# Optimization experiments

Hardware: AMD Instinct MI355X
Metric: run time of the kernel (lower is better)

The kernel has to match this reference:

```python
import jax, jax.numpy as jnp
import numpy as np

C = 1.0          # curvature
TOP_K = 5
LAMBDA_H = 0.01
TAU = 0.1        # forward default
NEG_SAMPLES = 20 # forward default
EPS = 1e-9
B, D = 4096, 64


def _to_ball(v):
    # map gaussian vectors strictly inside the unit Poincare ball
    return 0.8 * v / (1.0 + jnp.linalg.norm(v, axis=-1, keepdims=True))


def setup_inputs() -> dict:
    key = jax.random.key(0)
    ka, kt = jax.random.split(key)
    audio = _to_ball(jax.random.normal(ka, (B, D), dtype=jnp.float32))
    text = _to_ball(jax.random.normal(kt, (B, D), dtype=jnp.float32))
    return {"audio_embeds": audio, "text_embeds": text}


def _pairwise_poincare(x, y, c=C):
    # ||x-y||^2 via gemm instead of materializing [N,N,D] diff tensor
    x_sq = jnp.sum(x * x, axis=-1, keepdims=True)          # [N,1]
    y_sq = jnp.sum(y * y, axis=-1, keepdims=True).T        # [1,M]
    diff_sq = jnp.maximum(x_sq + y_sq - 2.0 * (x @ y.T), 0.0)
    x_cl = jnp.minimum(x_sq, 1.0 - EPS)
    y_cl = jnp.minimum(y_sq, 1.0 - EPS)
    denom = jnp.maximum((1.0 - x_cl) * (1.0 - y_cl), EPS)
    z = jnp.maximum(1.0 + 2.0 * diff_sq / denom, 1.0 + EPS)
    return jnp.arccosh(z) / jnp.sqrt(jnp.asarray(c, x.dtype))


def _topk_triplet(embeds, key):
    n = embeds.shape[0]
    dist = _pairwise_poincare(embeds, embeds)
    dist = dist.at[jnp.arange(n), jnp.arange(n)].set(jnp.inf)  # fill_diagonal_(inf)
    k = min(TOP_K, n - 1)
    neg_pos, pos_idx = jax.lax.top_k(-dist, k)                 # k smallest distances
    pos_term = jax.scipy.special.logsumexp(neg_pos / TAU, axis=1)  # logsumexp(-pos_dist/tau)
    # mask out top-k positives (diagonal stays in pool, holding +inf -> exp(-inf)=0)
    mask = jnp.ones((n, n), bool).at[jnp.arange(n)[:, None], pos_idx].set(False)
    # stable argsort: mask-True columns first, in original column order -> matches dist[i][mask[i]]
    order = jnp.argsort(jnp.where(mask, 0, 1), axis=1)
    pool = jnp.take_along_axis(dist, order[:, : n - k], axis=1)    # [n, n-k]
    samp = jax.random.randint(key, (n, NEG_SAMPLES), 0, n - k)
    neg_vals = jnp.take_along_axis(pool, samp, axis=1)             # [n, NEG_SAMPLES]
    neg_term = jax.scipy.special.logsumexp(-neg_vals / TAU, axis=1)
    return jnp.mean(neg_term - pos_term)  # mean of -(pos_term - neg_term)


def reference(audio_embeds, text_embeds):
    # HyperbolicLayeredLoss.forward returns lambda_h * (text_h + audio_h);
    # the cross-modal loss is computed but NOT added to the returned total in the source.
    key_text = jax.random.key(1)
    key_audio = jax.random.key(2)
    loss_text_h = _topk_triplet(text_embeds, key_text)
    loss_audio_h = _topk_triplet(audio_embeds, key_audio)
    return LAMBDA_H * (loss_text_h + loss_audio_h)
```

## Files before the change

kernel.cpp:

```cpp
#include <hip/hip_runtime.h>
#include <stdint.h>

#define JAX_PARTITIONABLE 1

constexpr int N = 4096;
constexpr int DIM = 64;
constexpr int TOPK = 5;
constexpr int NEGS = 20;
constexpr float TAU_ = 0.1f;
constexpr uint32_t SPAN = 4091u;
constexpr uint32_t MULT = 2309u;

constexpr int CQ = 256;
constexpr int NQ = N / CQ;
constexpr int NT = CQ / 16;
constexpr int RPB = 64;
constexpr int YSTRIDE = 136;

typedef __attribute__((ext_vector_type(8))) short bf16x8;
typedef __attribute__((ext_vector_type(4))) float f32x4;

__device__ __forceinline__ uint32_t rotl32(uint32_t v, int d) {
  return (v << d) | (v >> (32 - d));
}

__device__ __forceinline__ void threefry(uint32_t k0, uint32_t k1,
                                         uint32_t& x0, uint32_t& x1) {
  const uint32_t k2 = k0 ^ k1 ^ 0x1BD11BDAu;
  x0 += k0; x1 += k1;
#define TF_R(r) { x0 += x1; x1 = rotl32(x1, r); x1 ^= x0; }
  TF_R(13) TF_R(15) TF_R(26) TF_R(6)
  x0 += k1; x1 += k2 + 1u;
  TF_R(17) TF_R(29) TF_R(16) TF_R(24)
  x0 += k2; x1 += k0 + 2u;
  TF_R(13) TF_R(15) TF_R(26) TF_R(6)
  x0 += k0; x1 += k1 + 3u;
  TF_R(17) TF_R(29) TF_R(16) TF_R(24)
  x0 += k1; x1 += k2 + 4u;
  TF_R(13) TF_R(15) TF_R(26) TF_R(6)
  x0 += k2; x1 += k0 + 5u;
#undef TF_R
}

__device__ __forceinline__ uint32_t sample_idx(uint32_t seed, uint32_t f) {
#if JAX_PARTITIONABLE
  uint32_t a0 = 0u, a1 = 0u; threefry(0u, seed, a0, a1);
  uint32_t b0 = 0u, b1 = 1u; threefry(0u, seed, b0, b1);
  uint32_t h0 = 0u, h1 = f;  threefry(a0, a1, h0, h1);
  const uint32_t hi = h0 ^ h1;
  uint32_t l0 = 0u, l1 = f;  threefry(b0, b1, l0, l1);
  const uint32_t lo = l0 ^ l1;
#else
  uint32_t a0 = 0u, a1 = 2u; threefry(0u, seed, a0, a1);
  uint32_t c0 = 1u, c1 = 3u; threefry(0u, seed, c0, c1);
  const uint32_t HALF = (uint32_t)(N * NEGS / 2);
  uint32_t hi, lo;
  if (f < HALF) {
    uint32_t x0 = f, x1 = f + HALF; threefry(a0, c0, x0, x1); hi = x0;
    x0 = f; x1 = f + HALF;          threefry(a1, c1, x0, x1); lo = x0;
  } else {
    uint32_t x0 = f - HALF, x1 = f; threefry(a0, c0, x0, x1); hi = x1;
    x0 = f - HALF; x1 = f;          threefry(a1, c1, x0, x1); lo = x1;
  }
#endif
  return ((hi % SPAN) * MULT + (lo % SPAN)) % SPAN;
}

__device__ __forceinline__ float acosh_dev(float z) {
  return logf(z + sqrtf((z - 1.0f) * (z + 1.0f)));
}

__device__ __forceinline__ uint16_t f2bf(float f) {
  const uint32_t u = __float_as_uint(f);
  return (uint16_t)((u + 0x7FFFu + ((u >> 16) & 1u)) >> 16);
}
__device__ __forceinline__ float bf2f(uint16_t h) {
  return __uint_as_float((uint32_t)h << 16);
}

__global__ __launch_bounds__(64) void k_pre(const float* __restrict__ Xa,
                                            const float* __restrict__ Xt,
                                            uint16_t* __restrict__ Xs,
                                            float* __restrict__ ysq,
                                            float* __restrict__ inv) {
  const int m = blockIdx.y;
  const float* __restrict__ X = (m == 0) ? Xt : Xa;
  const int i = blockIdx.x * 64 + threadIdx.x;
  const float* xr = X + (size_t)i * DIM;

  uint32_t hb[DIM / 2], lb[DIM / 2];
  float s = 0.0f;
#pragma unroll
  for (int u = 0; u < DIM / 4; ++u) {
    const float4 v = *(const float4*)(xr + 4 * u);
    s = fmaf(v.x, v.x, s); s = fmaf(v.y, v.y, s);
    s = fmaf(v.z, v.z, s); s = fmaf(v.w, v.w, s);
    const uint16_t h0 = f2bf(v.x), h1 = f2bf(v.y), h2 = f2bf(v.z), h3 = f2bf(v.w);
    const uint16_t l0 = f2bf(v.x - bf2f(h0)), l1 = f2bf(v.y - bf2f(h1));
    const uint16_t l2 = f2bf(v.z - bf2f(h2)), l3 = f2bf(v.w - bf2f(h3));
    hb[2 * u]     = (uint32_t)h0 | ((uint32_t)h1 << 16);
    hb[2 * u + 1] = (uint32_t)h2 | ((uint32_t)h3 << 16);
    lb[2 * u]     = (uint32_t)l0 | ((uint32_t)l1 << 16);
    lb[2 * u + 1] = (uint32_t)l2 | ((uint32_t)l3 << 16);
  }
  uint32_t* dst = (uint32_t*)(Xs + (size_t)(m * N + i) * 128);
#pragma unroll
  for (int w = 0; w < 8; ++w) {
    uint4 qh = { hb[4 * w], hb[4 * w + 1], hb[4 * w + 2], hb[4 * w + 3] };
    ((uint4*)dst)[w] = qh;
  }
#pragma unroll
  for (int w = 0; w < 8; ++w) {
    uint4 ql = { lb[4 * w], lb[4 * w + 1], lb[4 * w + 2], lb[4 * w + 3] };
    ((uint4*)dst)[8 + w] = ql;
  }
  ysq[m * N + i] = s;
  inv[m * N + i] = 1.0f / (1.0f - fminf(s, 1.0f));
}

__global__ __launch_bounds__(256) void k_top5(
    const uint16_t* __restrict__ Xs, const float* __restrict__ ysq,
    const float* __restrict__ inv, uint64_t* __restrict__ partial) {
  const int lin = (int)blockIdx.x;
  const int wg = ((lin & 7) << 8) | (lin >> 3);
  const int m = wg >> 10;
  const int qq = (wg >> 6) & 15;
  const int rb = wg & 63;

  const int tid = (int)threadIdx.x;
  const int wid = tid >> 6;
  const int l = tid & 63;
  const int i0w = rb * RPB + wid * 16;
  const int j0q = qq * CQ;
  const int mN = m * N;
  const uint16_t* __restrict__ Xm = Xs + (size_t)m * N * 128;
  const int lc = l & 15;
  const int lk = l >> 4;
  const int lk4 = lk * 4;
  const int lk8 = lk * 8;
  const int sr = tid >> 4;
  const int sc8 = (tid & 15) * 8;

  __shared__ __align__(16) unsigned char smem[2 * 16 * YSTRIDE * 2 + 2048];
  uint16_t* y0 = (uint16_t*)smem;
  uint16_t* y1 = y0 + 16 * YSTRIDE;
  float* sq_s = (float*)(smem + 2 * 16 * YSTRIDE * 2);
  float* iv_s = sq_s + CQ;

  bf16x8 xf[2][2];
#pragma unroll
  for (int c = 0; c < 2; ++c)
#pragma unroll
    for (int h = 0; h < 2; ++h)
      xf[c][h] = *(const bf16x8*)(Xm + (size_t)(i0w + lc) * 128 +
                                  h * 64 + c * 32 + lk8);

  const float xsq_i = ysq[mN + i0w + lc];
  const float inv2_i = 2.0f * inv[mN + i0w + lc];
  const int gi = i0w + lc;

  const uint64_t SENT = ((uint64_t)0x7F800000u << 32) | 0xFFFFFFFFu;
  uint64_t t5[TOPK];
#pragma unroll
  for (int t = 0; t < TOPK; ++t) t5[t] = SENT;

  const f32x4 zz = {0.0f, 0.0f, 0.0f, 0.0f};
  const float INF_ = __uint_as_float(0x7F800000u);

  {
    if (tid < 64)
      *(float4*)&sq_s[tid * 4] = *(const float4*)&ysq[mN + j0q + tid * 4];
    else if (tid < 128)
      *(float4*)&iv_s[(tid - 64) * 4] =
          *(const float4*)&inv[mN + j0q + (tid - 64) * 4];
    const uint4 s0 =
        *(const uint4*)(Xm + (size_t)(j0q + sr) * 128 + sc8);
    *(uint4*)(y0 + sr * YSTRIDE + sc8) = s0;
    __syncthreads();
  }

#pragma unroll 1
  for (int T = 0; T < NT; ++T) {
    const bool have_next = (T + 1 < NT);
    uint4 stg;
    if (have_next)
      stg = *(const uint4*)(Xm + (size_t)(j0q + (T + 1) * 16 + sr) * 128 + sc8);

    const uint16_t* yp = ((T & 1) ? y1 : y0) + lc * YSTRIDE + lk8;
    const bf16x8 Y0 = *(const bf16x8*)(yp);
    const bf16x8 Y1 = *(const bf16x8*)(yp + 32);
    const bf16x8 Y2 = *(const bf16x8*)(yp + 64);
    const bf16x8 Y3 = *(const bf16x8*)(yp + 96);

    f32x4 acc;
    acc = __builtin_amdgcn_mfma_f32_16x16x32_bf16(Y0, xf[0][0], zz, 0, 0, 0);
    acc = __builtin_amdgcn_mfma_f32_16x16x32_bf16(Y1, xf[1][0], acc, 0, 0, 0);
    acc = __builtin_amdgcn_mfma_f32_16x16x32_bf16(Y2, xf[0][0], acc, 0, 0, 0);
    acc = __builtin_amdgcn_mfma_f32_16x16x32_bf16(Y3, xf[1][0], acc, 0, 0, 0);
    acc = __builtin_amdgcn_mfma_f32_16x16x32_bf16(Y0, xf[0][1], acc, 0, 0, 0);
    acc = __builtin_amdgcn_mfma_f32_16x16x32_bf16(Y1, xf[1][1], acc, 0, 0, 0);

    const float4 sq4 = *(const float4*)&sq_s[T * 16 + lk4];
    const float4 iv4 = *(const float4*)&iv_s[T * 16 + lk4];
    const int jb = j0q + T * 16;

    float w_ = __uint_as_float((uint32_t)(t5[TOPK - 1] >> 32));
    w_ = fminf(w_, __shfl_xor(w_, 16, 64));
    const float tau_ = fminf(w_, __shfl_xor(w_, 32, 64));

    float zt[4];
#pragma unroll
    for (int p = 0; p < 4; ++p) {
      const float yc = (p == 0) ? sq4.x : (p == 1) ? sq4.y
                      : (p == 2) ? sq4.z : sq4.w;
      const float ic = (p == 0) ? iv4.x : (p == 1) ? iv4.y
                      : (p == 2) ? iv4.z : iv4.w;
      const float diff = fmaxf(xsq_i + yc - 2.0f * acc[p], 0.0f);
      zt[p] = fmaf(diff * inv2_i, ic, 1.0f);
    }
    if (jb == i0w) {
#pragma unroll
      for (int p = 0; p < 4; ++p)
        if (gi == jb + lk4 + p) zt[p] = INF_;
    }
    const float zm = fminf(fminf(zt[0], zt[1]), fminf(zt[2], zt[3]));
    if (zm <= tau_) {
#pragma unroll
      for (int p = 0; p < 4; ++p) {
        uint64_t key = ((uint64_t)__float_as_uint(zt[p]) << 32) |
                       (uint32_t)(jb + lk4 + p);
        if (key < t5[TOPK - 1]) {
#pragma unroll
          for (int tt = 0; tt < TOPK; ++tt) {
            const uint64_t cv = t5[tt];
            if (key < cv) { t5[tt] = key; key = cv; }
          }
        }
      }
    }

    if (have_next)
      *(uint4*)(((T & 1) ? y0 : y1) + sr * YSTRIDE + sc8) = stg;
    __syncthreads();
  }

  uint64_t* mb = (uint64_t*)smem;
#pragma unroll
  for (int t = 0; t < TOPK; ++t)
    mb[((size_t)(wid * 16) + lc) * 21 + lk * TOPK + t] = t5[t];
  __syncthreads();

  if (l < 16) {
    uint64_t cur[TOPK];
#pragma unroll
    for (int t = 0; t < TOPK; ++t) cur[t] = mb[((size_t)(wid * 16) + l) * 21 + t];
    for (int c = 1; c < 4; ++c) {
      for (int t = 0; t < TOPK; ++t) {
        uint64_t key = mb[((size_t)(wid * 16) + l) * 21 + c * TOPK + t];
        if (key >= cur[TOPK - 1]) break;
#pragma unroll
        for (int u = 0; u < TOPK; ++u) {
          const uint64_t cv = cur[u];
          if (key < cv) { cur[u] = key; key = cv; }
        }
      }
    }
#pragma unroll
    for (int t = 0; t < TOPK; ++t)
      partial[((size_t)(m * NQ + qq) * N + i0w + l) * TOPK + t] = cur[t];
  }
}

__global__ __launch_bounds__(64) void k_neg(const float* __restrict__ Xa,
                                            const float* __restrict__ Xt,
                                            const float* __restrict__ ysq,
                                            const float* __restrict__ inv,
                                            const uint64_t* __restrict__ partial,
                                            float* __restrict__ rowres) {
  const int m = blockIdx.y;
  const int i = blockIdx.x;
  const float* __restrict__ X = (m == 0) ? Xt : Xa;
  const uint32_t seed = (m == 0) ? 1u : 2u;
  const int lane = threadIdx.x;

  __shared__ float4 xi4[DIM / 4];
  __shared__ float posv[TOPK];
  if (lane < DIM / 4) xi4[lane] = ((const float4*)(X + (size_t)i * DIM))[lane];
  __syncthreads();

  uint64_t cur[TOPK];
#pragma unroll
  for (int t = 0; t < TOPK; ++t)
    cur[t] = partial[((size_t)(m * NQ) * N + i) * TOPK + t];
  for (int q = 1; q < NQ; ++q) {
    for (int t = 0; t < TOPK; ++t) {
      uint64_t key = partial[((size_t)(m * NQ + q) * N + i) * TOPK + t];
      if (key >= cur[TOPK - 1]) break;
#pragma unroll
      for (int u = 0; u < TOPK; ++u) {
        const uint64_t cv = cur[u];
        if (key < cv) { cur[u] = key; key = cv; }
      }
    }
  }

  const float ysq_i = ysq[m * N + i];
  const float inv_i = inv[m * N + i];

  if (lane >= 32 && lane < 32 + TOPK) {
    const int t = lane - 32;
    const uint32_t c = (uint32_t)(cur[t] & 0xffffffffu);
    const float4* xc = (const float4*)(X + (size_t)c * DIM);
    float dot = 0.0f;
#pragma unroll
    for (int k = 0; k < DIM / 4; ++k) {
      const float4 a = xi4[k];
      const float4 b = xc[k];
      dot = fmaf(a.x, b.x, dot); dot = fmaf(a.y, b.y, dot);
      dot = fmaf(a.z, b.z, dot); dot = fmaf(a.w, b.w, dot);
    }
    const float diff = fmaxf(ysq_i + ysq[m * N + c] - 2.0f * dot, 0.0f);
    const float z = 1.0f + 2.0f * diff * inv_i * inv[m * N + c];
    posv[t] = -acosh_dev(z) / TAU_;
  }

  uint32_t pidx[TOPK];
#pragma unroll
  for (int t = 0; t < TOPK; ++t) pidx[t] = (uint32_t)(cur[t] & 0xffffffffu);

#define CSWAP(a, b)                                                           \
  { const uint32_t mn = pidx[a] < pidx[b] ? pidx[a] : pidx[b];                \
    const uint32_t mx = pidx[a] < pidx[b] ? pidx[b] : pidx[a];                \
    pidx[a] = mn; pidx[b] = mx; }
  CSWAP(0, 1) CSWAP(3, 4) CSWAP(2, 4) CSWAP(2, 3) CSWAP(1, 4)
  CSWAP(0, 3) CSWAP(0, 2) CSWAP(1, 3) CSWAP(1, 2)
#undef CSWAP

  float v = -1e30f;
  if (lane < NEGS) {
    const uint32_t f = (uint32_t)i * (uint32_t)NEGS + (uint32_t)lane;
    uint32_t c = sample_idx(seed, f);
#pragma unroll
    for (int t = 0; t < TOPK; ++t) c += (c >= pidx[t]) ? 1u : 0u;
    if (c != (uint32_t)i) {
      const float4* xc = (const float4*)(X + (size_t)c * DIM);
      float dot = 0.0f;
#pragma unroll
      for (int k = 0; k < DIM / 4; ++k) {
        const float4 a = xi4[k];
        const float4 b = xc[k];
        dot = fmaf(a.x, b.x, dot); dot = fmaf(a.y, b.y, dot);
        dot = fmaf(a.z, b.z, dot); dot = fmaf(a.w, b.w, dot);
      }
      const float diff = fmaxf(ysq_i + ysq[m * N + c] - 2.0f * dot, 0.0f);
      const float z = 1.0f + 2.0f * diff * inv_i * inv[m * N + c];
      v = -acosh_dev(z) / TAU_;
    }
  }

  __syncthreads();

  float vmax = v;
#pragma unroll
  for (int o = 32; o > 0; o >>= 1) vmax = fmaxf(vmax, __shfl_xor(vmax, o, 64));
  float e = expf(v - vmax);
  float ss = e;
#pragma unroll
  for (int o = 32; o > 0; o >>= 1) ss += __shfl_xor(ss, o, 64);

  if (lane == 0) {
    float vm = -1e30f;
#pragma unroll
    for (int t = 0; t < TOPK; ++t) vm = fmaxf(vm, posv[t]);
    float ps = 0.0f;
#pragma unroll
    for (int t = 0; t < TOPK; ++t) ps += expf(posv[t] - vm);
    const float pos = vm + logf(ps);
    rowres[m * N + i] = (vmax + logf(ss)) - pos;
  }
}

__global__ __launch_bounds__(256) void k_reduce(const float* __restrict__ rowres,
                                                float* __restrict__ out) {
  __shared__ double sh[256];
  double s = 0.0;
  for (int idx = threadIdx.x; idx < 2 * N; idx += 256) s += (double)rowres[idx];
  sh[threadIdx.x] = s;
  __syncthreads();
  for (int o = 128; o > 0; o >>= 1) {
    if (threadIdx.x < o) sh[threadIdx.x] += sh[threadIdx.x + o];
    __syncthreads();
  }
  if (threadIdx.x == 0) out[0] = (float)(0.01 * (sh[0] / (double)N));
}

extern "C" void kernel_launch(void* const* d_in, const int* in_sizes, int n_in,
                              void* d_out, int out_size, void* d_ws,
                              size_t ws_size, hipStream_t stream) {
  const float* Xa = (const float*)d_in[0];
  const float* Xt = (const float*)d_in[1];
  float* out = (float*)d_out;

  float* ysq = (float*)d_ws;
  float* inv = ysq + 2 * N;
  uint64_t* partial = (uint64_t*)(inv + 2 * N);
  float* rowres = (float*)(partial + (size_t)2 * NQ * N * TOPK);
  uint16_t* Xs = (uint16_t*)(rowres + 2 * N);

  k_pre<<<dim3(N / 64, 2), 64, 0, stream>>>(Xa, Xt, Xs, ysq, inv);
  k_top5<<<(N / RPB) * NQ * 2, 256, 0, stream>>>(Xs, ysq, inv, partial);
  k_neg<<<dim3(N, 2), 64, 0, stream>>>(Xa, Xt, ysq, inv, partial, rowres);
  k_reduce<<<1, 256, 0, stream>>>(rowres, out);
}
```

Measured before the change: 107.1 us.

## Process two Y tiles per barrier and use per-lane top-k threshold

Grows the shared-memory Y staging from two to four 16-row buffers so each loop iteration handles two tiles and prefetches the next two, halving the number of __syncthreads calls. It also replaces the cross-lane shuffle-reduced pruning threshold with a per-lane threshold that is updated only after insertions, which removes two shuffles per tile. A per-lane threshold is looser than the min across lanes, so more candidates may reach the insertion sort. The larger LDS footprint could also lower occupancy.

```diff
diff --git a/kernel.cpp b/kernel.cpp
--- a/kernel.cpp
+++ b/kernel.cpp
@@ -141,10 +141,9 @@
   const int sr = tid >> 4;
   const int sc8 = (tid & 15) * 8;
 
-  __shared__ __align__(16) unsigned char smem[2 * 16 * YSTRIDE * 2 + 2048];
-  uint16_t* y0 = (uint16_t*)smem;
-  uint16_t* y1 = y0 + 16 * YSTRIDE;
-  float* sq_s = (float*)(smem + 2 * 16 * YSTRIDE * 2);
+  __shared__ __align__(16) unsigned char smem[4 * 16 * YSTRIDE * 2 + 2048];
+  uint16_t* ybuf = (uint16_t*)smem;
+  float* sq_s = (float*)(smem + 4 * 16 * YSTRIDE * 2);
   float* iv_s = sq_s + CQ;
 
   bf16x8 xf[2][2];
@@ -163,6 +162,7 @@
   uint64_t t5[TOPK];
 #pragma unroll
   for (int t = 0; t < TOPK; ++t) t5[t] = SENT;
+  float z5own = __uint_as_float(0x7F800000u);
 
   const f32x4 zz = {0.0f, 0.0f, 0.0f, 0.0f};
   const float INF_ = __uint_as_float(0x7F800000u);
@@ -173,76 +173,76 @@
     else if (tid < 128)
       *(float4*)&iv_s[(tid - 64) * 4] =
           *(const float4*)&inv[mN + j0q + (tid - 64) * 4];
-    const uint4 s0 =
+    *(uint4*)(ybuf + sr * YSTRIDE + sc8) =
         *(const uint4*)(Xm + (size_t)(j0q + sr) * 128 + sc8);
-    *(uint4*)(y0 + sr * YSTRIDE + sc8) = s0;
+    *(uint4*)(ybuf + 16 * YSTRIDE + sr * YSTRIDE + sc8) =
+        *(const uint4*)(Xm + (size_t)(j0q + 16 + sr) * 128 + sc8);
     __syncthreads();
   }
 
+#define PROCESS(T, BUF)                                                        \
+  {                                                                            \
+    const uint16_t* yp = (BUF) + lc * YSTRIDE + lk8;                           \
+    const bf16x8 Y0 = *(const bf16x8*)(yp);                                    \
+    const bf16x8 Y1 = *(const bf16x8*)(yp + 32);                               \
+    const bf16x8 Y2 = *(const bf16x8*)(yp + 64);                               \
+    const bf16x8 Y3 = *(const bf16x8*)(yp + 96);                               \
+    f32x4 acc;                \
+    acc = __builtin_amdgcn_mfma_f32_16x16x32_bf16(Y0, xf[0][0], zz, 0, 0, 0);  \
+    acc = __builtin_amdgcn_mfma_f32_16x16x32_bf16(Y1, xf[1][0], acc, 0, 0, 0); \
+    acc = __builtin_amdgcn_mfma_f32_16x16x32_bf16(Y2, xf[0][0], acc, 0, 0, 0); \
+    acc = __builtin_amdgcn_mfma_f32_16x16x32_bf16(Y3, xf[1][0], acc, 0, 0, 0); \
+    acc = __builtin_amdgcn_mfma_f32_16x16x32_bf16(Y0, xf[0][1], acc, 0, 0, 0); \
+    acc = __builtin_amdgcn_mfma_f32_16x16x32_bf16(Y1, xf[1][1], acc, 0, 0, 0); \
+    const float4 sq4 = *(const float4*)&sq_s[(T) * 16 + lk4];                  \
+    const float4 iv4 = *(const float4*)&iv_s[(T) * 16 + lk4];                  \
+    const int jb = j0q + (T) * 16;                                             \
+    float zt[4];                                                               \
+    _Pragma("unroll") for (int p = 0; p < 4; ++p) {                            \
+      const float yc = (p == 0) ? sq4.x : (p == 1) ? sq4.y                     \
+                      : (p == 2) ? sq4.z : sq4.w;                              \
+      const float ic = (p == 0) ? iv4.x : (p == 1) ? iv4.y                     \
+                      : (p == 2) ? iv4.z : iv4.w;                              \
+      const float diff = fmaxf(xsq_i + yc - 2.0f * acc[p], 0.0f);              \
+      zt[p] = fmaf(diff * inv2_i, ic, 1.0f);                                   \
+    }                                                                          \
+    if (jb == i0w) {                           \
+      _Pragma("unroll") for (int p = 0; p < 4; ++p)                            \
+        if (gi == jb + lk4 + p) zt[p] = INF_;                                  \
+    }                                                                          \
+    const float zm = fminf(fminf(zt[0], zt[1]), fminf(zt[2], zt[3]));          \
+    if (zm <= z5own) {                                                         \
+      _Pragma("unroll") for (int p = 0; p < 4; ++p) {                          \
+        uint64_t key = ((uint64_t)__float_as_uint(zt[p]) << 32) |              \
+                       (uint32_t)(jb + lk4 + p);                               \
+        if (key < t5[TOPK - 1]) {                                              \
+          _Pragma("unroll") for (int tt = 0; tt < TOPK; ++tt) {                \
+            const uint64_t cv = t5[tt];                                        \
+            if (key < cv) { t5[tt] = key; key = cv; }                          \
+          }                                                                    \
+        }                                                                      \
+      }                                                                        \
+      z5own = __uint_as_float((uint32_t)(t5[TOPK - 1] >> 32));                 \
+    }                                                                          \
+  }
+
 #pragma unroll 1
-  for (int T = 0; T < NT; ++T) {
-    const bool have_next = (T + 1 < NT);
-    uint4 stg;
-    if (have_next)
-      stg = *(const uint4*)(Xm + (size_t)(j0q + (T + 1) * 16 + sr) * 128 + sc8);
-
-    const uint16_t* yp = ((T & 1) ? y1 : y0) + lc * YSTRIDE + lk8;
-    const bf16x8 Y0 = *(const bf16x8*)(yp);
-    const bf16x8 Y1 = *(const bf16x8*)(yp + 32);
-    const bf16x8 Y2 = *(const bf16x8*)(yp + 64);
-    const bf16x8 Y3 = *(const bf16x8*)(yp + 96);
-
-    f32x4 acc;
-    acc = __builtin_amdgcn_mfma_f32_16x16x32_bf16(Y0, xf[0][0], zz, 0, 0, 0);
-    acc = __builtin_amdgcn_mfma_f32_16x16x32_bf16(Y1, xf[1][0], acc, 0, 0, 0);
-    acc = __builtin_amdgcn_mfma_f32_16x16x32_bf16(Y2, xf[0][0], acc, 0, 0, 0);
-    acc = __builtin_amdgcn_mfma_f32_16x16x32_bf16(Y3, xf[1][0], acc, 0, 0, 0);
-    acc = __builtin_amdgcn_mfma_f32_16x16x32_bf16(Y0, xf[0][1], acc, 0, 0, 0);
-    acc = __builtin_amdgcn_mfma_f32_16x16x32_bf16(Y1, xf[1][1], acc, 0, 0, 0);
-
-    const float4 sq4 = *(const float4*)&sq_s[T * 16 + lk4];
-    const float4 iv4 = *(const float4*)&iv_s[T * 16 + lk4];
-    const int jb = j0q + T * 16;
-
-    float w_ = __uint_as_float((uint32_t)(t5[TOPK - 1] >> 32));
-    w_ = fminf(w_, __shfl_xor(w_, 16, 64));
-    const float tau_ = fminf(w_, __shfl_xor(w_, 32, 64));
-
-    float zt[4];
-#pragma unroll
-    for (int p = 0; p < 4; ++p) {
-      const float yc = (p == 0) ? sq4.x : (p == 1) ? sq4.y
-                      : (p == 2) ? sq4.z : sq4.w;
-      const float ic = (p == 0) ? iv4.x : (p == 1) ? iv4.y
-                      : (p == 2) ? iv4.z : iv4.w;
-      const float diff = fmaxf(xsq_i + yc - 2.0f * acc[p], 0.0f);
-      zt[p] = fmaf(diff * inv2_i, ic, 1.0f);
-    }
-    if (jb == i0w) {
-#pragma unroll
-      for (int p = 0; p < 4; ++p)
-        if (gi == jb + lk4 + p) zt[p] = INF_;
-    }
-    const float zm = fminf(fminf(zt[0], zt[1]), fminf(zt[2], zt[3]));
-    if (zm <= tau_) {
-#pragma unroll
-      for (int p = 0; p < 4; ++p) {
-        uint64_t key = ((uint64_t)__float_as_uint(zt[p]) << 32) |
-                       (uint32_t)(jb + lk4 + p);
-        if (key < t5[TOPK - 1]) {
-#pragma unroll
-          for (int tt = 0; tt < TOPK; ++tt) {
-            const uint64_t cv = t5[tt];
-            if (key < cv) { t5[tt] = key; key = cv; }
-          }
-        }
-      }
-    }
-
-    if (have_next)
-      *(uint4*)(((T & 1) ? y0 : y1) + sr * YSTRIDE + sc8) = stg;
+  for (int T = 0; T < NT; T += 2) {
+    const bool hn = (T + 2 < NT);
+    uint4 s2, s3;
+    if (hn) {
+      s2 = *(const uint4*)(Xm + (size_t)(j0q + (T + 2) * 16 + sr) * 128 + sc8);
+      s3 = *(const uint4*)(Xm + (size_t)(j0q + (T + 3) * 16 + sr) * 128 + sc8);
+    }
+    PROCESS(T, ybuf + (size_t)((T) & 3) * 16 * YSTRIDE)
+    PROCESS(T + 1, ybuf + (size_t)((T + 1) & 3) * 16 * YSTRIDE)
+    if (hn) {
+      *(uint4*)(ybuf + (size_t)((T + 2) & 3) * 16 * YSTRIDE + sr * YSTRIDE + sc8) = s2;
+      *(uint4*)(ybuf + (size_t)((T + 3) & 3) * 16 * YSTRIDE + sr * YSTRIDE + sc8) = s3;
+    }
     __syncthreads();
   }
+#undef PROCESS
 
   uint64_t* mb = (uint64_t*)smem;
 #pragma unroll
```

New measurement: 104.8 us. -2.1%, faster.
